# Optimization experiments

Hardware: AMD Instinct MI355X
Metric: run time of the kernel (lower is better)

The kernel has to match this reference:

```python
import jax, jax.numpy as jnp
import numpy as np
import math

NUM_HEADS = 8
EMBED = 512
D_K = EMBED // NUM_HEADS
B, T1, T2 = 16, 512, 512
N_POS = 2 * T1 - 1


def rel_shift(x, left_context=0):
    # x: (B, H, T1, 2*T1-1) -> (B, H, T1, T2), out[i, j] = x[i, j - i + T1 - 1]
    t1 = x.shape[2]
    t2 = t1 + left_context
    idx = jnp.arange(t2)[None, :] - jnp.arange(t1)[:, None] + (t1 - 1)  # (T1, T2)
    return jnp.take_along_axis(x, idx[None, None, :, :], axis=-1)


def setup_inputs() -> dict:
    key = jax.random.key(0)
    ks = jax.random.split(key, 16)
    scale = 1.0 / math.sqrt(EMBED)
    inp = {
        "query": jax.random.normal(ks[0], (B, T1, EMBED), jnp.float32),
        "key": jax.random.normal(ks[1], (B, T2, EMBED), jnp.float32),
        "value": jax.random.normal(ks[2], (B, T2, EMBED), jnp.float32),
        "pos_enc": jax.random.normal(ks[3], (B, N_POS, EMBED), jnp.float32),
        "mask": jnp.zeros((B, T2), dtype=bool),
        "chunk_mask": jnp.zeros((T1, T1), dtype=bool),
        "Wq": jax.random.normal(ks[4], (EMBED, EMBED), jnp.float32) * scale,
        "bq": jnp.zeros((EMBED,), jnp.float32),
        "Wk": jax.random.normal(ks[5], (EMBED, EMBED), jnp.float32) * scale,
        "bk": jnp.zeros((EMBED,), jnp.float32),
        "Wv": jax.random.normal(ks[6], (EMBED, EMBED), jnp.float32) * scale,
        "bv": jnp.zeros((EMBED,), jnp.float32),
        "Wpos": jax.random.normal(ks[7], (EMBED, EMBED), jnp.float32) * scale,
        "Wo": jax.random.normal(ks[8], (EMBED, EMBED), jnp.float32) * scale,
        "bo": jnp.zeros((EMBED,), jnp.float32),
        "pos_bias_u": jax.random.normal(ks[9], (NUM_HEADS, D_K), jnp.float32) * 0.1,
        "pos_bias_v": jax.random.normal(ks[10], (NUM_HEADS, D_K), jnp.float32) * 0.1,
        "left_context": 0,
    }
    return inp


def reference(query, key, value, pos_enc, mask, chunk_mask, Wq, bq, Wk, bk, Wv, bv,
              Wpos, Wo, bo, pos_bias_u, pos_bias_v, left_context):
    b, t1, _ = query.shape
    t2 = key.shape[1]
    # qkv projections -> (B, T, H, d_k)
    q = (query @ Wq.T + bq).reshape(b, t1, NUM_HEADS, D_K)
    k = (key @ Wk.T + bk).reshape(b, t2, NUM_HEADS, D_K)
    v = (value @ Wv.T + bv).reshape(b, t2, NUM_HEADS, D_K)
    # positional projection (no bias) -> (B, N, H, d_k)
    p = (pos_enc @ Wpos.T).reshape(b, -1, NUM_HEADS, D_K)
    # content and positional scores
    matrix_ac = jnp.einsum('bihd,bjhd->bhij', q + pos_bias_u, k)  # (B,H,T1,T2)
    matrix_bd = jnp.einsum('bihd,bnhd->bhin', q + pos_bias_v, p)  # (B,H,T1,N)
    matrix_bd = rel_shift(matrix_bd, left_context=left_context)   # (B,H,T1,T2)
    scores = (matrix_ac + matrix_bd) / math.sqrt(D_K)
    # combined mask: True = masked
    m = chunk_mask[None, None, :, :] | mask[:, None, None, :]
    neg_inf = jnp.finfo(scores.dtype).min
    scores = jnp.where(m, neg_inf, scores)
    attn = jax.nn.softmax(scores, axis=-1)
    attn = jnp.where(m, 0.0, attn)
    out = jnp.einsum('bhij,bjhd->bihd', attn, v).reshape(b, t1, NUM_HEADS * D_K)
    return out @ Wo.T + bo
```

## Files before the change

kernel.cpp:

```cpp
#include <hip/hip_runtime.h>
#include <math.h>

typedef _Float16 f16;
typedef f16 f16x8 __attribute__((ext_vector_type(8)));
typedef f16 f16x4 __attribute__((ext_vector_type(4)));
typedef float f32x4 __attribute__((ext_vector_type(4)));

#define H_   8
#define E_   512
#define DK   64
#define BB   16
#define T1C  512
#define T2C  512
#define NPOS 1023

struct CastDesc {
    const float* src[9];
    f16* dst[9];
    int nsrc[9];
    int ndst[9];
};
__global__ __launch_bounds__(256) void cast_f32_f16(CastDesc cd) {
    const int s = blockIdx.y;
    const float* sp = cd.src[s];
    f16* dp = cd.dst[s];
    const int n4 = cd.ndst[s] >> 2;
    const int ns = cd.nsrc[s];
    for (int i = blockIdx.x * 256 + threadIdx.x; i < n4; i += gridDim.x * 256) {
        const int base = i * 4;
        float4 v = make_float4(0.f, 0.f, 0.f, 0.f);
        if (base < ns) v = *(const float4*)(sp + base);
        f16x4 h; h[0] = (f16)v.x; h[1] = (f16)v.y; h[2] = (f16)v.z; h[3] = (f16)v.w;
        *(f16x4*)(dp + base) = h;
    }
}

struct PArg {
    const f16* A; const f16* W; const float* bias; const float* bias2;
    void* C; int Mvalid; int mode;
};
struct PArgs { PArg g[4]; };

__device__ __forceinline__ void gemm64_body(const PArg g, int bx, int by) {
    __shared__ f16 Al[64 * 40];
    __shared__ f16 Wl[64 * 40];
    const int tid = threadIdx.x;
    const int lane = tid & 63, w = tid >> 6;
    const int quad = lane >> 4, l15 = lane & 15;
    const int m0 = by * 64, n0 = bx * 64;
    const int row = tid >> 2, koff = (tid & 3) * 8;

    f32x4 acc[4];
    #pragma unroll
    for (int nt = 0; nt < 4; ++nt) acc[nt] = (f32x4){0.f, 0.f, 0.f, 0.f};

    const size_t aoff = (size_t)(m0 + row) * 512;
    const size_t woff = (size_t)(n0 + row) * 512;

    for (int k0 = 0; k0 < 512; k0 += 32) {
        const uint4 av = *(const uint4*)&g.A[aoff + k0 + koff];
        const uint4 wv = *(const uint4*)&g.W[woff + k0 + koff];
        __syncthreads();
        *(uint4*)&Al[row * 40 + koff] = av;
        *(uint4*)&Wl[row * 40 + koff] = wv;
        __syncthreads();
        const f16x8 af = *(const f16x8*)&Al[(w * 16 + l15) * 40 + quad * 8];
        #pragma unroll
        for (int nt = 0; nt < 4; ++nt) {
            const f16x8 bf = *(const f16x8*)&Wl[(nt * 16 + l15) * 40 + quad * 8];
            acc[nt] = __builtin_amdgcn_mfma_f32_16x16x32_f16(af, bf, acc[nt], 0, 0, 0);
        }
    }

    const int mb = m0 + w * 16 + quad * 4;
    #pragma unroll
    for (int nt = 0; nt < 4; ++nt) {
        const int n = n0 + nt * 16 + l15;
        const f32x4 a = acc[nt];
        float bs = g.bias ? g.bias[n] : 0.f;
        if (g.bias2) bs += g.bias2[n];
        if (g.mode == 0) {
            float* C = (float*)g.C;
            #pragma unroll
            for (int r = 0; r < 4; ++r) C[(size_t)(mb + r) * 512 + n] = a[r] + bs;
        } else if (g.mode == 1) {
            f16* C = (f16*)g.C;
            const int b = mb >> 9, t = mb & 511;
            const int hh = n >> 6, dk = n & 63;
            f16x4 h;
            #pragma unroll
            for (int r = 0; r < 4; ++r) h[r] = (f16)(a[r] + bs);
            *(f16x4*)&C[(((size_t)b * H_ + hh) * DK + dk) * 512 + t] = h;
        } else if (g.mode == 2) {
            f16* C = (f16*)g.C;
            const int b = mb >> 9, t = mb & 511;
            const int hh = n >> 6, dk = n & 63;
            #pragma unroll
            for (int r = 0; r < 4; ++r)
                C[(((size_t)b * H_ + hh) * 512 + t + r) * DK + dk] = (f16)(a[r] + bs);
        } else {
            f16* C = (f16*)g.C;
            const int hh = n >> 6, dk = n & 63;
            #pragma unroll
            for (int r = 0; r < 4; ++r) {
                const int m = mb + r;
                if (m < g.Mvalid) {
                    const int b = m / NPOS, t = m - b * NPOS;
                    C[(((size_t)b * H_ + hh) * NPOS + t) * DK + dk] = (f16)a[r];
                }
            }
        }
    }
}

__global__ __launch_bounds__(256) void proj_all(PArgs a) {
    const int id = blockIdx.x;
    int gi, rem;
    if (id < 3072) { gi = id >> 10; rem = id & 1023; }
    else           { gi = 3;        rem = id - 3072; }
    gemm64_body(a.g[gi], rem & 7, rem >> 3);
}
__global__ __launch_bounds__(256) void proj_one(PArg g) {
    gemm64_body(g, blockIdx.x & 7, blockIdx.x >> 3);
}

__global__ __launch_bounds__(256) void attn_mfma(
    const f16* __restrict__ Qh,
    const f16* __restrict__ Kh,
    const f16* __restrict__ Vt,
    const f16* __restrict__ Ph,
    const float* __restrict__ pbu, const float* __restrict__ pbv,
    const unsigned char* __restrict__ bmask,
    const unsigned char* __restrict__ cmask,
    f16* __restrict__ CTX)
{
    __shared__ f16 Qa[64 * 72];
    __shared__ f16 Ka[64 * 72];
    __shared__ f16 Va[64 * 72];
    __shared__ f16 Pa[128 * 72];
    __shared__ unsigned char Ma[64 * 64];

    const int tid = threadIdx.x;
    const int lane = tid & 63, w = tid >> 6;
    const int quad = lane >> 4, l15 = lane & 15;
    const int it = blockIdx.x, h = blockIdx.y, b = blockIdx.z;
    const int i0 = it * 64;
    const int bh = b * H_ + h;
    const int rowt = w * 16 + quad * 4;

    #pragma unroll
    for (int rep = 0; rep < 2; ++rep) {
        const int flat = rep * 2048 + tid * 8;
        const int r = flat >> 6, c = flat & 63;
        *(uint4*)&Qa[r * 72 + c] = *(const uint4*)&Qh[((size_t)bh * 512 + i0 + r) * 64 + c];
    }
    f16x8 dpbf[2];
    #pragma unroll
    for (int ks = 0; ks < 2; ++ks)
        #pragma unroll
        for (int j = 0; j < 8; ++j) {
            const int d = ks * 32 + quad * 8 + j;
            dpbf[ks][j] = (f16)(pbv[h * 64 + d] - pbu[h * 64 + d]);
        }

    float m_run[4], l_run[4];
    f32x4 accO[4];
    #pragma unroll
    for (int x = 0; x < 4; ++x) {
        m_run[x] = -__builtin_inff(); l_run[x] = 0.f;
        accO[x] = (f32x4){0.f, 0.f, 0.f, 0.f};
    }

    const int mr = tid >> 2, mc = (tid & 3) * 16;

    for (int jt = 0; jt < 8; ++jt) {
        const int j0 = jt * 64;
        const int nbase = j0 - i0 + 448;
        __syncthreads();
        #pragma unroll
        for (int rep = 0; rep < 2; ++rep) {
            const int flat = rep * 2048 + tid * 8;
            const int r = flat >> 6, c = flat & 63;
            *(uint4*)&Ka[r * 72 + c] = *(const uint4*)&Kh[((size_t)bh * 512 + j0 + r) * 64 + c];
            *(uint4*)&Va[r * 72 + c] = *(const uint4*)&Vt[((size_t)bh * 64 + r) * 512 + j0 + c];
        }
        #pragma unroll
        for (int rep = 0; rep < 4; ++rep) {
            const int flat = rep * 2048 + tid * 8;
            const int nw = flat >> 6, c = flat & 63;
            int n = nbase + nw; n = n > (NPOS - 1) ? (NPOS - 1) : n;
            *(uint4*)&Pa[nw * 72 + c] = *(const uint4*)&Ph[((size_t)bh * NPOS + n) * 64 + c];
        }
        {
            const uint4 cm = *(const uint4*)&cmask[(size_t)(i0 + mr) * 512 + j0 + mc];
            const uint4 bm = *(const uint4*)&bmask[(size_t)b * 512 + j0 + mc];
            uint4 mm;
            mm.x = cm.x | bm.x; mm.y = cm.y | bm.y;
            mm.z = cm.z | bm.z; mm.w = cm.w | bm.w;
            *(uint4*)&Ma[mr * 64 + mc] = mm;
        }
        __syncthreads();

        f16x8 afQ[2], afV[2];
        #pragma unroll
        for (int ks = 0; ks < 2; ++ks) {
            afQ[ks] = *(const f16x8*)&Qa[(w * 16 + l15) * 72 + ks * 32 + quad * 8];
            afV[ks] = afQ[ks] + dpbf[ks];
        }
        f32x4 accAC[4];
        #pragma unroll
        for (int nt = 0; nt < 4; ++nt) {
            accAC[nt] = (f32x4){0.f, 0.f, 0.f, 0.f};
            #pragma unroll
            for (int ks = 0; ks < 2; ++ks) {
                const f16x8 bf = *(const f16x8*)&Ka[(nt * 16 + l15) * 72 + ks * 32 + quad * 8];
                accAC[nt] = __builtin_amdgcn_mfma_f32_16x16x32_f16(afQ[ks], bf, accAC[nt], 0, 0, 0);
            }
        }
        f32x4 accBD[5];
        #pragma unroll
        for (int u = 0; u < 5; ++u) {
            accBD[u] = (f32x4){0.f, 0.f, 0.f, 0.f};
            const int nts = (3 - w) + u;
            #pragma unroll
            for (int ks = 0; ks < 2; ++ks) {
                const f16x8 bf = *(const f16x8*)&Pa[(nts * 16 + l15) * 72 + ks * 32 + quad * 8];
                accBD[u] = __builtin_amdgcn_mfma_f32_16x16x32_f16(afV[ks], bf, accBD[u], 0, 0, 0);
            }
        }
        __syncthreads();

        #pragma unroll
        for (int rg = 0; rg < 4; ++rg) {
            const int qr = quad * 4 + rg;
            const int rt = rowt + rg;
            float tmpv[5];
            #pragma unroll
            for (int u = 0; u < 5; ++u) {
                const int cl = l15 + (3 + u) * 16 + qr - 63;
                const int dst = (quad * 16 + (cl & 15)) << 2;
                tmpv[u] = __uint_as_float(
                    (unsigned)__builtin_amdgcn_ds_permute(dst, (int)__float_as_uint(accBD[u][rg])));
            }
            const bool hi = l15 > qr;
            float sv[4]; unsigned mk = 0;
            #pragma unroll
            for (int nt = 0; nt < 4; ++nt) {
                const int c = nt * 16 + l15;
                const float bdv = hi ? tmpv[nt + 1] : tmpv[nt];
                float s = (accAC[nt][rg] + bdv) * 0.125f;
                if (Ma[rt * 64 + c]) { s = -3.402823466e38f; mk |= 1u << nt; }
                sv[nt] = s;
            }
            float tmax = fmaxf(fmaxf(sv[0], sv[1]), fmaxf(sv[2], sv[3]));
            #pragma unroll
            for (int d = 1; d < 16; d <<= 1) tmax = fmaxf(tmax, __shfl_xor(tmax, d));
            const float mnew = fmaxf(m_run[rg], tmax);
            const float alpha = __expf(m_run[rg] - mnew);
            float rsum = 0.f;
            f16 wv[4];
            #pragma unroll
            for (int nt = 0; nt < 4; ++nt) {
                const float e = __expf(sv[nt] - mnew);
                rsum += e;
                wv[nt] = ((mk >> nt) & 1u) ? (f16)0.f : (f16)e;
            }
            #pragma unroll
            for (int d = 1; d < 16; d <<= 1) rsum += __shfl_xor(rsum, d);
            l_run[rg] = l_run[rg] * alpha + rsum;
            m_run[rg] = mnew;
            #pragma unroll
            for (int dt = 0; dt < 4; ++dt) accO[dt][rg] *= alpha;
            #pragma unroll
            for (int nt = 0; nt < 4; ++nt)
                Ka[rt * 72 + nt * 16 + l15] = wv[nt];
        }
        f16x8 afW[2];
        #pragma unroll
        for (int ks = 0; ks < 2; ++ks)
            afW[ks] = *(const f16x8*)&Ka[(w * 16 + l15) * 72 + ks * 32 + quad * 8];
        #pragma unroll
        for (int dt = 0; dt < 4; ++dt)
            #pragma unroll
            for (int ks = 0; ks < 2; ++ks) {
                const f16x8 bf = *(const f16x8*)&Va[(dt * 16 + l15) * 72 + ks * 32 + quad * 8];
                accO[dt] = __builtin_amdgcn_mfma_f32_16x16x32_f16(afW[ks], bf, accO[dt], 0, 0, 0);
            }
    }

    #pragma unroll
    for (int rg = 0; rg < 4; ++rg) {
        const float inv = 1.0f / l_run[rg];
        const int gi = i0 + rowt + rg;
        #pragma unroll
        for (int dt = 0; dt < 4; ++dt)
            CTX[((size_t)b * 512 + gi) * 512 + h * 64 + dt * 16 + l15] = (f16)(accO[dt][rg] * inv);
    }
}

extern "C" void kernel_launch(void* const* d_in, const int* in_sizes, int n_in,
                              void* d_out, int out_size, void* d_ws, size_t ws_size,
                              hipStream_t stream) {
    const float* query   = (const float*)d_in[0];
    const float* key     = (const float*)d_in[1];
    const float* value   = (const float*)d_in[2];
    const float* pos_enc = (const float*)d_in[3];
    const unsigned char* mask       = (const unsigned char*)d_in[4];
    const unsigned char* chunk_mask = (const unsigned char*)d_in[5];
    const float* Wq  = (const float*)d_in[6];
    const float* bq  = (const float*)d_in[7];
    const float* Wk  = (const float*)d_in[8];
    const float* bk  = (const float*)d_in[9];
    const float* Wv  = (const float*)d_in[10];
    const float* bv  = (const float*)d_in[11];
    const float* Wpos = (const float*)d_in[12];
    const float* Wo   = (const float*)d_in[13];
    const float* bo   = (const float*)d_in[14];
    const float* pbu  = (const float*)d_in[15];
    const float* pbv  = (const float*)d_in[16];
    float* out = (float*)d_out;

    f16* base = (f16*)d_ws;
    size_t off = 0;
    f16* qh  = base + off; off += 4194304;
    f16* kh  = base + off; off += 4194304;
    f16* vh  = base + off; off += 4194304;
    f16* ph  = base + off; off += 8388608;
    f16* wqh = base + off; off += 262144;
    f16* wkh = base + off; off += 262144;
    f16* wvh = base + off; off += 262144;
    f16* wph = base + off; off += 262144;
    f16* woh = base + off; off += 262144;
    f16* ctx = base + off; off += 4194304;
    f16* Qhm = base + off; off += 4194304;
    f16* Khm = base + off; off += 4194304;
    f16* Vtm = base + off; off += 4194304;
    f16* Phm = base + off; off += 8380416;

    CastDesc cd;
    cd.src[0] = query;   cd.dst[0] = qh;  cd.nsrc[0] = 4194304; cd.ndst[0] = 4194304;
    cd.src[1] = key;     cd.dst[1] = kh;  cd.nsrc[1] = 4194304; cd.ndst[1] = 4194304;
    cd.src[2] = value;   cd.dst[2] = vh;  cd.nsrc[2] = 4194304; cd.ndst[2] = 4194304;
    cd.src[3] = pos_enc; cd.dst[3] = ph;  cd.nsrc[3] = 8380416; cd.ndst[3] = 8388608;
    cd.src[4] = Wq;   cd.dst[4] = wqh; cd.nsrc[4] = 262144; cd.ndst[4] = 262144;
    cd.src[5] = Wk;   cd.dst[5] = wkh; cd.nsrc[5] = 262144; cd.ndst[5] = 262144;
    cd.src[6] = Wv;   cd.dst[6] = wvh; cd.nsrc[6] = 262144; cd.ndst[6] = 262144;
    cd.src[7] = Wpos; cd.dst[7] = wph; cd.nsrc[7] = 262144; cd.ndst[7] = 262144;
    cd.src[8] = Wo;   cd.dst[8] = woh; cd.nsrc[8] = 262144; cd.ndst[8] = 262144;
    cast_f32_f16<<<dim3(256, 9), 256, 0, stream>>>(cd);

    PArgs pa;
    pa.g[0] = PArg{qh, wqh, bq, pbu,     (void*)Qhm, 8192,  2};
    pa.g[1] = PArg{kh, wkh, bk, nullptr, (void*)Khm, 8192,  2};
    pa.g[2] = PArg{vh, wvh, bv, nullptr, (void*)Vtm, 8192,  1};
    pa.g[3] = PArg{ph, wph, nullptr, nullptr, (void*)Phm, 16368, 3};
    proj_all<<<dim3(5120), 256, 0, stream>>>(pa);

    attn_mfma<<<dim3(8, 8, 16), 256, 0, stream>>>(Qhm, Khm, Vtm, Phm, pbu, pbv,
                                                  mask, chunk_mask, ctx);

    PArg go = PArg{ctx, woh, bo, nullptr, (void*)out, 8192, 0};
    proj_one<<<dim3(1024), 256, 0, stream>>>(go);
}
```

Measured before the change: 320.1 us.

## Fuse fp32-to-fp16 casts into projection GEMMs and prefetch attention tiles

Removes the separate cast kernel and its fp16 intermediate buffers. The projection GEMMs now load fp32 activations and weights directly and convert them in registers before writing to LDS. Both the GEMM loop and the attention loop now prefetch the next tile's global loads into registers while the current tile computes, overlapping memory latency with MFMA work. The cost is more register pressure and twice the global read volume for the fp32 weights, which every block now re-reads and converts.

Result: no change. 316.6 us (-1.1%).

```diff
diff --git a/kernel.cpp b/kernel.cpp
--- a/kernel.cpp
+++ b/kernel.cpp
@@ -14,30 +14,16 @@
 #define T2C  512
 #define NPOS 1023
 
-struct CastDesc {
-    const float* src[9];
-    f16* dst[9];
-    int nsrc[9];
-    int ndst[9];
-};
-__global__ __launch_bounds__(256) void cast_f32_f16(CastDesc cd) {
-    const int s = blockIdx.y;
-    const float* sp = cd.src[s];
-    f16* dp = cd.dst[s];
-    const int n4 = cd.ndst[s] >> 2;
-    const int ns = cd.nsrc[s];
-    for (int i = blockIdx.x * 256 + threadIdx.x; i < n4; i += gridDim.x * 256) {
-        const int base = i * 4;
-        float4 v = make_float4(0.f, 0.f, 0.f, 0.f);
-        if (base < ns) v = *(const float4*)(sp + base);
-        f16x4 h; h[0] = (f16)v.x; h[1] = (f16)v.y; h[2] = (f16)v.z; h[3] = (f16)v.w;
-        *(f16x4*)(dp + base) = h;
-    }
+__device__ __forceinline__ f16x8 cvt8(const float4 a, const float4 b) {
+    f16x8 h;
+    h[0] = (f16)a.x; h[1] = (f16)a.y; h[2] = (f16)a.z; h[3] = (f16)a.w;
+    h[4] = (f16)b.x; h[5] = (f16)b.y; h[6] = (f16)b.z; h[7] = (f16)b.w;
+    return h;
 }
 
 struct PArg {
-    const f16* A; const f16* W; const float* bias; const float* bias2;
-    void* C; int Mvalid; int mode;
+    const void* A; const float* W; const float* bias; const float* bias2;
+    void* C; int Mvalid; int mode; int a16;
 };
 struct PArgs { PArg g[4]; };
 
@@ -49,21 +35,42 @@
     const int quad = lane >> 4, l15 = lane & 15;
     const int m0 = by * 64, n0 = bx * 64;
     const int row = tid >> 2, koff = (tid & 3) * 8;
+    int arow = m0 + row; if (arow >= g.Mvalid) arow = g.Mvalid - 1;
+    const size_t aoff = (size_t)arow * 512 + koff;
+    const size_t woff = (size_t)(n0 + row) * 512 + koff;
 
     f32x4 acc[4];
     #pragma unroll
     for (int nt = 0; nt < 4; ++nt) acc[nt] = (f32x4){0.f, 0.f, 0.f, 0.f};
 
-    const size_t aoff = (size_t)(m0 + row) * 512;
-    const size_t woff = (size_t)(n0 + row) * 512;
-
-    for (int k0 = 0; k0 < 512; k0 += 32) {
-        const uint4 av = *(const uint4*)&g.A[aoff + k0 + koff];
-        const uint4 wv = *(const uint4*)&g.W[woff + k0 + koff];
-        __syncthreads();
-        *(uint4*)&Al[row * 40 + koff] = av;
-        *(uint4*)&Wl[row * 40 + koff] = wv;
-        __syncthreads();
+    float4 fa0, fa1, fw0, fw1;
+    uint4 ha;
+    if (g.a16) {
+        ha = *(const uint4*)((const f16*)g.A + aoff);
+    } else {
+        fa0 = *(const float4*)((const float*)g.A + aoff);
+        fa1 = *(const float4*)((const float*)g.A + aoff + 4);
+    }
+    fw0 = *(const float4*)(g.W + woff);
+    fw1 = *(const float4*)(g.W + woff + 4);
+
+    for (int ki = 0; ki < 16; ++ki) {
+        __syncthreads();
+        if (g.a16) *(uint4*)&Al[row * 40 + koff] = ha;
+        else       *(f16x8*)&Al[row * 40 + koff] = cvt8(fa0, fa1);
+        *(f16x8*)&Wl[row * 40 + koff] = cvt8(fw0, fw1);
+        __syncthreads();
+        if (ki < 15) {
+            const int k0 = (ki + 1) * 32;
+            if (g.a16) {
+                ha = *(const uint4*)((const f16*)g.A + aoff + k0);
+            } else {
+                fa0 = *(const float4*)((const float*)g.A + aoff + k0);
+                fa1 = *(const float4*)((const float*)g.A + aoff + k0 + 4);
+            }
+            fw0 = *(const float4*)(g.W + woff + k0);
+            fw1 = *(const float4*)(g.W + woff + k0 + 4);
+        }
         const f16x8 af = *(const f16x8*)&Al[(w * 16 + l15) * 40 + quad * 8];
         #pragma unroll
         for (int nt = 0; nt < 4; ++nt) {
@@ -147,13 +154,12 @@
     const int i0 = it * 64;
     const int bh = b * H_ + h;
     const int rowt = w * 16 + quad * 4;
-
-    #pragma unroll
-    for (int rep = 0; rep < 2; ++rep) {
-        const int flat = rep * 2048 + tid * 8;
-        const int r = flat >> 6, c = flat & 63;
-        *(uint4*)&Qa[r * 72 + c] = *(const uint4*)&Qh[((size_t)bh * 512 + i0 + r) * 64 + c];
-    }
+    const int sr = tid >> 3, sc = (tid & 7) * 8;
+    const int mr = tid >> 2, mc = (tid & 3) * 16;
+
+    *(uint4*)&Qa[sr * 72 + sc] = *(const uint4*)&Qh[((size_t)bh * 512 + i0 + sr) * 64 + sc];
+    *(uint4*)&Qa[(sr + 32) * 72 + sc] =
+        *(const uint4*)&Qh[((size_t)bh * 512 + i0 + sr + 32) * 64 + sc];
     f16x8 dpbf[2];
     #pragma unroll
     for (int ks = 0; ks < 2; ++ks)
@@ -171,35 +177,58 @@
         accO[x] = (f32x4){0.f, 0.f, 0.f, 0.f};
     }
 
-    const int mr = tid >> 2, mc = (tid & 3) * 16;
+    uint4 pK0, pK1, pV0, pV1, pP0, pP1, pP2, pP3, pM;
+    {
+        const int j0 = 0, nbase = 448 - i0;
+        pK0 = *(const uint4*)&Kh[((size_t)bh * 512 + j0 + sr) * 64 + sc];
+        pK1 = *(const uint4*)&Kh[((size_t)bh * 512 + j0 + sr + 32) * 64 + sc];
+        pV0 = *(const uint4*)&Vt[((size_t)bh * 64 + sr) * 512 + j0 + sc];
+        pV1 = *(const uint4*)&Vt[((size_t)bh * 64 + sr + 32) * 512 + j0 + sc];
+        int n0_ = nbase + sr;       if (n0_ > NPOS - 1) n0_ = NPOS - 1;
+        int n1_ = nbase + sr + 32;  if (n1_ > NPOS - 1) n1_ = NPOS - 1;
+        int n2_ = nbase + sr + 64;  if (n2_ > NPOS - 1) n2_ = NPOS - 1;
+        int n3_ = nbase + sr + 96;  if (n3_ > NPOS - 1) n3_ = NPOS - 1;
+        pP0 = *(const uint4*)&Ph[((size_t)bh * NPOS + n0_) * 64 + sc];
+        pP1 = *(const uint4*)&Ph[((size_t)bh * NPOS + n1_) * 64 + sc];
+        pP2 = *(const uint4*)&Ph[((size_t)bh * NPOS + n2_) * 64 + sc];
+        pP3 = *(const uint4*)&Ph[((size_t)bh * NPOS + n3_) * 64 + sc];
+        const uint4 cm = *(const uint4*)&cmask[(size_t)(i0 + mr) * 512 + j0 + mc];
+        const uint4 bm = *(const uint4*)&bmask[(size_t)b * 512 + j0 + mc];
+        pM.x = cm.x | bm.x; pM.y = cm.y | bm.y; pM.z = cm.z | bm.z; pM.w = cm.w | bm.w;
+    }
 
     for (int jt = 0; jt < 8; ++jt) {
-        const int j0 = jt * 64;
-        const int nbase = j0 - i0 + 448;
-        __syncthreads();
-        #pragma unroll
-        for (int rep = 0; rep < 2; ++rep) {
-            const int flat = rep * 2048 + tid * 8;
-            const int r = flat >> 6, c = flat & 63;
-            *(uint4*)&Ka[r * 72 + c] = *(const uint4*)&Kh[((size_t)bh * 512 + j0 + r) * 64 + c];
-            *(uint4*)&Va[r * 72 + c] = *(const uint4*)&Vt[((size_t)bh * 64 + r) * 512 + j0 + c];
-        }
-        #pragma unroll
-        for (int rep = 0; rep < 4; ++rep) {
-            const int flat = rep * 2048 + tid * 8;
-            const int nw = flat >> 6, c = flat & 63;
-            int n = nbase + nw; n = n > (NPOS - 1) ? (NPOS - 1) : n;
-            *(uint4*)&Pa[nw * 72 + c] = *(const uint4*)&Ph[((size_t)bh * NPOS + n) * 64 + c];
-        }
-        {
-            const uint4 cm = *(const uint4*)&cmask[(size_t)(i0 + mr) * 512 + j0 + mc];
-            const uint4 bm = *(const uint4*)&bmask[(size_t)b * 512 + j0 + mc];
-            uint4 mm;
-            mm.x = cm.x | bm.x; mm.y = cm.y | bm.y;
-            mm.z = cm.z | bm.z; mm.w = cm.w | bm.w;
-            *(uint4*)&Ma[mr * 64 + mc] = mm;
-        }
-        __syncthreads();
+        __syncthreads();
+        *(uint4*)&Ka[sr * 72 + sc] = pK0;
+        *(uint4*)&Ka[(sr + 32) * 72 + sc] = pK1;
+        *(uint4*)&Va[sr * 72 + sc] = pV0;
+        *(uint4*)&Va[(sr + 32) * 72 + sc] = pV1;
+        *(uint4*)&Pa[sr * 72 + sc] = pP0;
+        *(uint4*)&Pa[(sr + 32) * 72 + sc] = pP1;
+        *(uint4*)&Pa[(sr + 64) * 72 + sc] = pP2;
+        *(uint4*)&Pa[(sr + 96) * 72 + sc] = pP3;
+        *(uint4*)&Ma[mr * 64 + mc] = pM;
+        __syncthreads();
+
+        if (jt < 7) {
+            const int j0n = (jt + 1) * 64;
+            const int nbase = j0n - i0 + 448;
+            pK0 = *(const uint4*)&Kh[((size_t)bh * 512 + j0n + sr) * 64 + sc];
+            pK1 = *(const uint4*)&Kh[((size_t)bh * 512 + j0n + sr + 32) * 64 + sc];
+            pV0 = *(const uint4*)&Vt[((size_t)bh * 64 + sr) * 512 + j0n + sc];
+            pV1 = *(const uint4*)&Vt[((size_t)bh * 64 + sr + 32) * 512 + j0n + sc];
+            int n0_ = nbase + sr;       if (n0_ > NPOS - 1) n0_ = NPOS - 1;
+            int n1_ = nbase + sr + 32;  if (n1_ > NPOS - 1) n1_ = NPOS - 1;
+            int n2_ = nbase + sr + 64;  if (n2_ > NPOS - 1) n2_ = NPOS - 1;
+            int n3_ = nbase + sr + 96;  if (n3_ > NPOS - 1) n3_ = NPOS - 1;
+            pP0 = *(const uint4*)&Ph[((size_t)bh * NPOS + n0_) * 64 + sc];
+            pP1 = *(const uint4*)&Ph[((size_t)bh * NPOS + n1_) * 64 + sc];
+            pP2 = *(const uint4*)&Ph[((size_t)bh * NPOS + n2_) * 64 + sc];
+            pP3 = *(const uint4*)&Ph[((size_t)bh * NPOS + n3_) * 64 + sc];
+            const uint4 cm = *(const uint4*)&cmask[(size_t)(i0 + mr) * 512 + j0n + mc];
+            const uint4 bm = *(const uint4*)&bmask[(size_t)b * 512 + j0n + mc];
+            pM.x = cm.x | bm.x; pM.y = cm.y | bm.y; pM.z = cm.z | bm.z; pM.w = cm.w | bm.w;
+        }
 
         f16x8 afQ[2], afV[2];
         #pragma unroll
@@ -322,43 +351,22 @@
 
     f16* base = (f16*)d_ws;
     size_t off = 0;
-    f16* qh  = base + off; off += 4194304;
-    f16* kh  = base + off; off += 4194304;
-    f16* vh  = base + off; off += 4194304;
-    f16* ph  = base + off; off += 8388608;
-    f16* wqh = base + off; off += 262144;
-    f16* wkh = base + off; off += 262144;
-    f16* wvh = base + off; off += 262144;
-    f16* wph = base + off; off += 262144;
-    f16* woh = base + off; off += 262144;
     f16* ctx = base + off; off += 4194304;
     f16* Qhm = base + off; off += 4194304;
     f16* Khm = base + off; off += 4194304;
     f16* Vtm = base + off; off += 4194304;
     f16* Phm = base + off; off += 8380416;
 
-    CastDesc cd;
-    cd.src[0] = query;   cd.dst[0] = qh;  cd.nsrc[0] = 4194304; cd.ndst[0] = 4194304;
-    cd.src[1] = key;     cd.dst[1] = kh;  cd.nsrc[1] = 4194304; cd.ndst[1] = 4194304;
-    cd.src[2] = value;   cd.dst[2] = vh;  cd.nsrc[2] = 4194304; cd.ndst[2] = 4194304;
-    cd.src[3] = pos_enc; cd.dst[3] = ph;  cd.nsrc[3] = 8380416; cd.ndst[3] = 8388608;
-    cd.src[4] = Wq;   cd.dst[4] = wqh; cd.nsrc[4] = 262144; cd.ndst[4] = 262144;
-    cd.src[5] = Wk;   cd.dst[5] = wkh; cd.nsrc[5] = 262144; cd.ndst[5] = 262144;
-    cd.src[6] = Wv;   cd.dst[6] = wvh; cd.nsrc[6] = 262144; cd.ndst[6] = 262144;
-    cd.src[7] = Wpos; cd.dst[7] = wph; cd.nsrc[7] = 262144; cd.ndst[7] = 262144;
-    cd.src[8] = Wo;   cd.dst[8] = woh; cd.nsrc[8] = 262144; cd.ndst[8] = 262144;
-    cast_f32_f16<<<dim3(256, 9), 256, 0, stream>>>(cd);
-
     PArgs pa;
-    pa.g[0] = PArg{qh, wqh, bq, pbu,     (void*)Qhm, 8192,  2};
-    pa.g[1] = PArg{kh, wkh, bk, nullptr, (void*)Khm, 8192,  2};
-    pa.g[2] = PArg{vh, wvh, bv, nullptr, (void*)Vtm, 8192,  1};
-    pa.g[3] = PArg{ph, wph, nullptr, nullptr, (void*)Phm, 16368, 3};
+    pa.g[0] = PArg{query,   Wq,   bq, pbu,     (void*)Qhm, 8192,  2, 0};
+    pa.g[1] = PArg{key,     Wk,   bk, nullptr, (void*)Khm, 8192,  2, 0};
+    pa.g[2] = PArg{value,   Wv,   bv, nullptr, (void*)Vtm, 8192,  1, 0};
+    pa.g[3] = PArg{pos_enc, Wpos, nullptr, nullptr, (void*)Phm, 16368, 3, 0};
     proj_all<<<dim3(5120), 256, 0, stream>>>(pa);
 
     attn_mfma<<<dim3(8, 8, 16), 256, 0, stream>>>(Qhm, Khm, Vtm, Phm, pbu, pbv,
                                                   mask, chunk_mask, ctx);
 
-    PArg go = PArg{ctx, woh, bo, nullptr, (void*)out, 8192, 0};
+    PArg go = PArg{ctx, Wo, bo, nullptr, (void*)out, 8192, 0, 1};
     proj_one<<<dim3(1024), 256, 0, stream>>>(go);
 }
```
